# Kernel tuning notes

Hardware: AMD Instinct MI355X
Metric: run time of the kernel (lower is better)

Reference implementation:

```python
import jax, jax.numpy as jnp
import numpy as np

L = 32768          # sequence length (keys/values)
E = 1024           # embed_dim (hardcoded in module via weight slices)
H, D = 8, 128      # num_heads, head_dim (hardcoded via reshape(-1, 8, 128))


def setup_inputs() -> dict:
    key = jax.random.key(0)
    k1, k2, k3, k4, k5 = jax.random.split(key, 5)
    scale = 1.0 / np.sqrt(E)
    return {
        "x": jax.random.normal(k1, (L, E), dtype=jnp.float32),
        "in_proj_weight": jax.random.normal(k2, (3 * E, E), dtype=jnp.float32) * scale,
        "in_proj_bias": jax.random.normal(k3, (3 * E,), dtype=jnp.float32) * 0.02,
        "out_proj_weight": jax.random.normal(k4, (E, E), dtype=jnp.float32) * scale,
        "out_proj_bias": jax.random.normal(k5, (E,), dtype=jnp.float32) * 0.02,
    }


def reference(x, in_proj_weight, in_proj_bias, out_proj_weight, out_proj_bias):
    # Single-query (decode-style) attention: q from first token only.
    q = x[:1] @ in_proj_weight[:E].T + in_proj_bias[:E]              # [1, E]
    k = x @ in_proj_weight[E:2 * E].T + in_proj_bias[E:2 * E]        # [L, E]
    v = x @ in_proj_weight[2 * E:].T + in_proj_bias[2 * E:]          # [L, E]

    q = q.reshape(-1, H, D).transpose(1, 0, 2)                       # [H, 1, D]
    k = k.reshape(-1, H, D).transpose(1, 2, 0)                       # [H, D, L]
    v = v.reshape(-1, H, D).transpose(1, 0, 2)                       # [H, L, D]

    dot = jnp.matmul(q, k) * (1.0 / np.sqrt(D))                      # [H, 1, L]
    attn = jax.nn.softmax(dot, axis=-1)
    out = jnp.matmul(attn, v)                                        # [H, 1, D]

    out = out.transpose(1, 0, 2).reshape(-1, E)                      # [1, E]
    out = out @ out_proj_weight.T + out_proj_bias                    # [1, E]
    return out
```

## Files before the change

### kernel.cpp

```cpp
#include <hip/hip_runtime.h>
#include <math.h>


#define L_SEQ   32768
#define E_DIM   1024
#define NHEAD   8
#define HDIM    128
#define TILE_R  16
#define WAVES_M 8

__global__ __launch_bounds__(256) void proj_q(
    const float* __restrict__ W, const float* __restrict__ bias,
    const float* __restrict__ x, float* __restrict__ q)
{
  const int t = threadIdx.x, wave = t >> 6, lane = t & 63;
  const int o = blockIdx.x * 4 + wave;
  const float4* Wr = (const float4*)(W + (size_t)o * E_DIM);
  const float4* xr = (const float4*)x;
  float a = 0.f;
#pragma unroll
  for (int k = 0; k < 4; ++k) {
    float4 wv = Wr[lane + 64 * k];
    float4 xv = xr[lane + 64 * k];
    a += wv.x * xv.x + wv.y * xv.y + wv.z * xv.z + wv.w * xv.w;
  }
#pragma unroll
  for (int m = 1; m < 64; m <<= 1) a += __shfl_xor(a, m, 64);
  if (lane == 0) q[o] = a + bias[o];
}

__global__ __launch_bounds__(128) void make_p(
    const float* __restrict__ W, const float* __restrict__ q,
    float* __restrict__ P_T)
{
  const int h = blockIdx.y;
  const int e = blockIdx.x * 128 + threadIdx.x;
  const float* qh = q + h * HDIM;
  const float* Wb = W + ((size_t)E_DIM + (size_t)h * HDIM) * E_DIM + e;
  float a0 = 0.f, a1 = 0.f, a2 = 0.f, a3 = 0.f;
#pragma unroll 4
  for (int d = 0; d < HDIM; d += 4) {
    a0 += qh[d + 0] * Wb[(size_t)(d + 0) * E_DIM];
    a1 += qh[d + 1] * Wb[(size_t)(d + 1) * E_DIM];
    a2 += qh[d + 2] * Wb[(size_t)(d + 2) * E_DIM];
    a3 += qh[d + 3] * Wb[(size_t)(d + 3) * E_DIM];
  }
  P_T[h * E_DIM + e] = ((a0 + a1) + (a2 + a3)) * 0.08838834764831845f;
}

__global__ __launch_bounds__(512, 4) void attn_fused3(
    const float* __restrict__ x,
    const float* __restrict__ P_T,
    float* __restrict__ partial_z,
    float* __restrict__ partial_sumw,
    int rows_per_blk)
{
  __shared__ __align__(16) float P_lds[NHEAD * E_DIM];
  __shared__ __align__(16) float w_tile[2][TILE_R][NHEAD];
  __shared__ __align__(16) float sw_stage[WAVES_M][NHEAD];

  const int t = threadIdx.x;
  const int wave = t >> 6;
  const int lane = t & 63;
  const size_t row0 = (size_t)blockIdx.x * rows_per_blk;
  const int ntiles = rows_per_blk >> 4;

  const int rr_l = lane & 1;
  const int h_l = (((lane >> 1) & 1) << 2) | (((lane >> 2) & 1) << 1) | ((lane >> 3) & 1);

  {
    const float4* src = (const float4*)P_T;
    float4* dst = (float4*)P_lds;
#pragma unroll
    for (int i = 0; i < 4; ++i) dst[i * 512 + t] = src[i * 512 + t];
  }
  __syncthreads();

  float acc[16];
#pragma unroll
  for (int i = 0; i < 16; ++i) acc[i] = 0.f;
  float sumw_own = 0.f;

  for (int tile = 0; tile < ntiles; ++tile) {
    const int buf = tile & 1;
    const size_t trow = row0 + (size_t)tile * TILE_R;

    {
      const float4* xra = (const float4*)(x + (trow + wave * 2 + 0) * E_DIM);
      const float4* xrb = (const float4*)(x + (trow + wave * 2 + 1) * E_DIM);
      float4 xva[4], xvb[4];
#pragma unroll
      for (int k = 0; k < 4; ++k) xva[k] = xra[lane + 64 * k];
#pragma unroll
      for (int k = 0; k < 4; ++k) xvb[k] = xrb[lane + 64 * k];

      float v[16];
#pragma unroll
      for (int h = 0; h < NHEAD; ++h) {
        const float4* pr = (const float4*)(P_lds + h * E_DIM);
        float a0 = 0.f, a1 = 0.f;
#pragma unroll
        for (int k = 0; k < 4; ++k) {
          float4 p = pr[lane + 64 * k];
          a0 += xva[k].x * p.x + xva[k].y * p.y + xva[k].z * p.z + xva[k].w * p.w;
          a1 += xvb[k].x * p.x + xvb[k].y * p.y + xvb[k].z * p.z + xvb[k].w * p.w;
        }
        v[h] = a0; v[8 + h] = a1;
      }

#pragma unroll
      for (int lev = 0; lev < 4; ++lev) {
        const int d = 1 << lev;
        const int half = 8 >> lev;
#pragma unroll
        for (int i = 0; i < half; ++i) {
          float lo = v[i], hi = v[i + half];
          float keep = (lane & d) ? hi : lo;
          float oth  = (lane & d) ? lo : hi;
          v[i] = keep + __shfl_xor(oth, d, 64);
        }
      }
      float tot = v[0];
      tot += __shfl_xor(tot, 16, 64);
      tot += __shfl_xor(tot, 32, 64);

      const float w = __expf(tot);
      sumw_own += w;
      if (lane < 16) w_tile[buf][wave * 2 + rr_l][h_l] = w;
    }
    __syncthreads();

    {
      const float* xb = x + trow * E_DIM + 2 * t;
#pragma unroll
      for (int r4 = 0; r4 < TILE_R; r4 += 4) {
        float2 xv2[4];
#pragma unroll
        for (int j = 0; j < 4; ++j) xv2[j] = *(const float2*)(xb + (size_t)(r4 + j) * E_DIM);
        float4 wlo[4], whi[4];
#pragma unroll
        for (int j = 0; j < 4; ++j) {
          const float4* wp = (const float4*)&w_tile[buf][r4 + j][0];
          wlo[j] = wp[0]; whi[j] = wp[1];
        }
#pragma unroll
        for (int j = 0; j < 4; ++j) {
          acc[0]  += wlo[j].x * xv2[j].x;  acc[1]  += wlo[j].x * xv2[j].y;
          acc[2]  += wlo[j].y * xv2[j].x;  acc[3]  += wlo[j].y * xv2[j].y;
          acc[4]  += wlo[j].z * xv2[j].x;  acc[5]  += wlo[j].z * xv2[j].y;
          acc[6]  += wlo[j].w * xv2[j].x;  acc[7]  += wlo[j].w * xv2[j].y;
          acc[8]  += whi[j].x * xv2[j].x;  acc[9]  += whi[j].x * xv2[j].y;
          acc[10] += whi[j].y * xv2[j].x;  acc[11] += whi[j].y * xv2[j].y;
          acc[12] += whi[j].z * xv2[j].x;  acc[13] += whi[j].z * xv2[j].y;
          acc[14] += whi[j].w * xv2[j].x;  acc[15] += whi[j].w * xv2[j].y;
        }
      }
    }
  }

  {
    float* zd = partial_z + (size_t)blockIdx.x * (NHEAD * E_DIM) + 2 * t;
#pragma unroll
    for (int h = 0; h < NHEAD; ++h)
      *(float2*)(zd + h * E_DIM) = make_float2(acc[2 * h], acc[2 * h + 1]);
  }

  {
    float s2 = sumw_own + __shfl_xor(sumw_own, 1, 64);
    if (lane < 16 && (lane & 1) == 0) sw_stage[wave][h_l] = s2;
  }
  __syncthreads();
  if (t < NHEAD) {
    float s = 0.f;
#pragma unroll
    for (int wv = 0; wv < WAVES_M; ++wv) s += sw_stage[wv][t];
    partial_sumw[blockIdx.x * NHEAD + t] = s;
  }
}

__global__ __launch_bounds__(256) void reduce_z(
    const float* __restrict__ partial_z,
    const float* __restrict__ partial_sumw,
    float* __restrict__ zn, int nblk)
{
  __shared__ float red[256];
  __shared__ __align__(16) float swst[4][NHEAD];
  __shared__ float sumw_s[NHEAD];
  const int t = threadIdx.x;
  const int lane = t & 63, wave = t >> 6;

  float sw[NHEAD];
#pragma unroll
  for (int h = 0; h < NHEAD; ++h) sw[h] = 0.f;
  for (int b = t; b < nblk; b += 256) {
    const float4* p = (const float4*)(partial_sumw + (size_t)b * NHEAD);
    float4 a0 = p[0], a1 = p[1];
    sw[0] += a0.x; sw[1] += a0.y; sw[2] += a0.z; sw[3] += a0.w;
    sw[4] += a1.x; sw[5] += a1.y; sw[6] += a1.z; sw[7] += a1.w;
  }
#pragma unroll
  for (int m = 1; m < 64; m <<= 1) {
#pragma unroll
    for (int h = 0; h < NHEAD; ++h) sw[h] += __shfl_xor(sw[h], m, 64);
  }
  if (lane == 0) {
#pragma unroll
    for (int h = 0; h < NHEAD; ++h) swst[wave][h] = sw[h];
  }
  __syncthreads();
  if (t < NHEAD) sumw_s[t] = swst[0][t] + swst[1][t] + swst[2][t] + swst[3][t];

  const int o = blockIdx.x * 32 + (t & 31);
  const int g = t >> 5;
  float a = 0.f;
  for (int b = g; b < nblk; b += 8) a += partial_z[(size_t)b * (NHEAD * E_DIM) + o];
  red[t] = a;
  __syncthreads();
  if (t < 32) {
    float s2 = 0.f;
#pragma unroll
    for (int gg = 0; gg < 8; ++gg) s2 += red[gg * 32 + t];
    const int oo = blockIdx.x * 32 + t;
    zn[oo] = s2 / sumw_s[oo >> 10];
  }
}

__global__ __launch_bounds__(256) void proj_v(
    const float* __restrict__ W, const float* __restrict__ bias,
    const float* __restrict__ zn, float* __restrict__ attn)
{
  const int t = threadIdx.x, wave = t >> 6, lane = t & 63;
  const int o = blockIdx.x * 4 + wave;
  const float4* Wr = (const float4*)(W + ((size_t)2 * E_DIM + o) * E_DIM);
  const float4* zr = (const float4*)(zn + (size_t)(o >> 7) * E_DIM);
  float a = 0.f;
#pragma unroll
  for (int k = 0; k < 4; ++k) {
    float4 wv = Wr[lane + 64 * k];
    float4 zv = zr[lane + 64 * k];
    a += wv.x * zv.x + wv.y * zv.y + wv.z * zv.z + wv.w * zv.w;
  }
#pragma unroll
  for (int m = 1; m < 64; m <<= 1) a += __shfl_xor(a, m, 64);
  if (lane == 0) attn[o] = a + bias[2 * E_DIM + o];
}

__global__ __launch_bounds__(256) void proj_o(
    const float* __restrict__ Wo, const float* __restrict__ bo,
    const float* __restrict__ attn, float* __restrict__ out)
{
  const int t = threadIdx.x, wave = t >> 6, lane = t & 63;
  const int o = blockIdx.x * 4 + wave;
  const float4* Wr = (const float4*)(Wo + (size_t)o * E_DIM);
  const float4* vr = (const float4*)attn;
  float a = 0.f;
#pragma unroll
  for (int k = 0; k < 4; ++k) {
    float4 wv = Wr[lane + 64 * k];
    float4 vv = vr[lane + 64 * k];
    a += wv.x * vv.x + wv.y * vv.y + wv.z * vv.z + wv.w * vv.w;
  }
#pragma unroll
  for (int m = 1; m < 64; m <<= 1) a += __shfl_xor(a, m, 64);
  if (lane == 0) out[o] = a + bo[o];
}

extern "C" void kernel_launch(void* const* d_in, const int* in_sizes, int n_in,
                              void* d_out, int out_size, void* d_ws, size_t ws_size,
                              hipStream_t stream)
{
  const float* x  = (const float*)d_in[0];
  const float* Wi = (const float*)d_in[1];
  const float* bi = (const float*)d_in[2];
  const float* Wo = (const float*)d_in[3];
  const float* bo = (const float*)d_in[4];
  float* out = (float*)d_out;

  const size_t hdr = 90112;
  int nblk = 128;
  if (ws_size >= hdr + (size_t)512 * NHEAD * E_DIM * 4) nblk = 512;
  else if (ws_size >= hdr + (size_t)256 * NHEAD * E_DIM * 4) nblk = 256;
  const int rows_per_blk = L_SEQ / nblk;

  char* ws = (char*)d_ws;
  float* q     = (float*)(ws + 0);
  float* P_T   = (float*)(ws + 4096);
  float* zn    = (float*)(ws + 36864);
  float* attn  = (float*)(ws + 69632);
  float* psumw = (float*)(ws + 73728);
  float* pz    = (float*)(ws + hdr);

  proj_q     <<<256, 256, 0, stream>>>(Wi, bi, x, q);
  make_p     <<<dim3(8, 8), 128, 0, stream>>>(Wi, q, P_T);
  attn_fused3<<<nblk, 512, 0, stream>>>(x, P_T, pz, psumw, rows_per_blk);
  reduce_z   <<<256, 256, 0, stream>>>(pz, psumw, zn, nblk);
  proj_v     <<<256, 256, 0, stream>>>(Wi, bi, zn, attn);
  proj_o     <<<256, 256, 0, stream>>>(Wo, bo, attn, out);
}
```

Baseline: 243.1 us.

## Split fused attention kernel into score and accumulate passes with row prefetch

The fused kernel that computed exp-scores and then accumulated weighted x per 16-row tile with a barrier in between is split into two kernels. The score pass writes per-row weights to a global buffer and prefetches the next rows of x into registers, and it has no per-tile block barrier. The accumulate pass loads those weights into LDS and streams x with no barriers. The cost is reading the 128 MB x twice from memory instead of once, plus one extra launch, in exchange for removing per-tile synchronisation stalls.

```diff
diff --git a/kernel.cpp b/kernel.cpp
--- a/kernel.cpp
+++ b/kernel.cpp
@@ -6,7 +6,6 @@
 #define E_DIM   1024
 #define NHEAD   8
 #define HDIM    128
-#define TILE_R  16
 #define WAVES_M 8
 
 __global__ __launch_bounds__(256) void proj_q(
@@ -48,22 +47,21 @@
   P_T[h * E_DIM + e] = ((a0 + a1) + (a2 + a3)) * 0.08838834764831845f;
 }
 
-__global__ __launch_bounds__(512, 4) void attn_fused3(
+__global__ __launch_bounds__(512, 4) void score_pass(
     const float* __restrict__ x,
     const float* __restrict__ P_T,
-    float* __restrict__ partial_z,
+    float* __restrict__ wbuf,
     float* __restrict__ partial_sumw,
     int rows_per_blk)
 {
   __shared__ __align__(16) float P_lds[NHEAD * E_DIM];
-  __shared__ __align__(16) float w_tile[2][TILE_R][NHEAD];
   __shared__ __align__(16) float sw_stage[WAVES_M][NHEAD];
 
   const int t = threadIdx.x;
   const int wave = t >> 6;
   const int lane = t & 63;
   const size_t row0 = (size_t)blockIdx.x * rows_per_blk;
-  const int ntiles = rows_per_blk >> 4;
+  const int iters = rows_per_blk >> 4;
 
   const int rr_l = lane & 1;
   const int h_l = (((lane >> 1) & 1) << 2) | (((lane >> 2) & 1) << 1) | ((lane >> 3) & 1);
@@ -76,93 +74,71 @@
   }
   __syncthreads();
 
-  float acc[16];
-#pragma unroll
-  for (int i = 0; i < 16; ++i) acc[i] = 0.f;
   float sumw_own = 0.f;
 
-  for (int tile = 0; tile < ntiles; ++tile) {
-    const int buf = tile & 1;
-    const size_t trow = row0 + (size_t)tile * TILE_R;
-
-    {
-      const float4* xra = (const float4*)(x + (trow + wave * 2 + 0) * E_DIM);
-      const float4* xrb = (const float4*)(x + (trow + wave * 2 + 1) * E_DIM);
-      float4 xva[4], xvb[4];
-#pragma unroll
-      for (int k = 0; k < 4; ++k) xva[k] = xra[lane + 64 * k];
-#pragma unroll
-      for (int k = 0; k < 4; ++k) xvb[k] = xrb[lane + 64 * k];
-
-      float v[16];
-#pragma unroll
-      for (int h = 0; h < NHEAD; ++h) {
-        const float4* pr = (const float4*)(P_lds + h * E_DIM);
-        float a0 = 0.f, a1 = 0.f;
-#pragma unroll
-        for (int k = 0; k < 4; ++k) {
-          float4 p = pr[lane + 64 * k];
-          a0 += xva[k].x * p.x + xva[k].y * p.y + xva[k].z * p.z + xva[k].w * p.w;
-          a1 += xvb[k].x * p.x + xvb[k].y * p.y + xvb[k].z * p.z + xvb[k].w * p.w;
-        }
-        v[h] = a0; v[8 + h] = a1;
+  float4 xva[4], xvb[4];
+  {
+    const size_t trow = row0 + wave * 2;
+    const float4* xra = (const float4*)(x + trow * E_DIM);
+    const float4* xrb = (const float4*)(x + (trow + 1) * E_DIM);
+#pragma unroll
+    for (int k = 0; k < 4; ++k) xva[k] = xra[lane + 64 * k];
+#pragma unroll
+    for (int k = 0; k < 4; ++k) xvb[k] = xrb[lane + 64 * k];
+  }
+
+  for (int it = 0; it < iters; ++it) {
+    const size_t trow = row0 + (size_t)it * 16 + wave * 2;
+
+    float4 xna[4], xnb[4];
+    if (it + 1 < iters) {
+      const size_t nrow = trow + 16;
+      const float4* xra = (const float4*)(x + nrow * E_DIM);
+      const float4* xrb = (const float4*)(x + (nrow + 1) * E_DIM);
+#pragma unroll
+      for (int k = 0; k < 4; ++k) xna[k] = xra[lane + 64 * k];
+#pragma unroll
+      for (int k = 0; k < 4; ++k) xnb[k] = xrb[lane + 64 * k];
+    }
+
+    float v[16];
+#pragma unroll
+    for (int h = 0; h < NHEAD; ++h) {
+      const float4* pr = (const float4*)(P_lds + h * E_DIM);
+      float a0 = 0.f, a1 = 0.f;
+#pragma unroll
+      for (int k = 0; k < 4; ++k) {
+        float4 p = pr[lane + 64 * k];
+        a0 += xva[k].x * p.x + xva[k].y * p.y + xva[k].z * p.z + xva[k].w * p.w;
+        a1 += xvb[k].x * p.x + xvb[k].y * p.y + xvb[k].z * p.z + xvb[k].w * p.w;
       }
-
-#pragma unroll
-      for (int lev = 0; lev < 4; ++lev) {
-        const int d = 1 << lev;
-        const int half = 8 >> lev;
-#pragma unroll
-        for (int i = 0; i < half; ++i) {
-          float lo = v[i], hi = v[i + half];
-          float keep = (lane & d) ? hi : lo;
-          float oth  = (lane & d) ? lo : hi;
-          v[i] = keep + __shfl_xor(oth, d, 64);
-        }
+      v[h] = a0; v[8 + h] = a1;
+    }
+
+#pragma unroll
+    for (int lev = 0; lev < 4; ++lev) {
+      const int d = 1 << lev;
+      const int half = 8 >> lev;
+#pragma unroll
+      for (int i = 0; i < half; ++i) {
+        float lo = v[i], hi = v[i + half];
+        float keep = (lane & d) ? hi : lo;
+        float oth  = (lane & d) ? lo : hi;
+        v[i] = keep + __shfl_xor(oth, d, 64);
       }
-      float tot = v[0];
-      tot += __shfl_xor(tot, 16, 64);
-      tot += __shfl_xor(tot, 32, 64);
-
-      const float w = __expf(tot);
-      sumw_own += w;
-      if (lane < 16) w_tile[buf][wave * 2 + rr_l][h_l] = w;
-    }
-    __syncthreads();
-
-    {
-      const float* xb = x + trow * E_DIM + 2 * t;
-#pragma unroll
-      for (int r4 = 0; r4 < TILE_R; r4 += 4) {
-        float2 xv2[4];
-#pragma unroll
-        for (int j = 0; j < 4; ++j) xv2[j] = *(const float2*)(xb + (size_t)(r4 + j) * E_DIM);
-        float4 wlo[4], whi[4];
-#pragma unroll
-        for (int j = 0; j < 4; ++j) {
-          const float4* wp = (const float4*)&w_tile[buf][r4 + j][0];
-          wlo[j] = wp[0]; whi[j] = wp[1];
-        }
-#pragma unroll
-        for (int j = 0; j < 4; ++j) {
-          acc[0]  += wlo[j].x * xv2[j].x;  acc[1]  += wlo[j].x * xv2[j].y;
-          acc[2]  += wlo[j].y * xv2[j].x;  acc[3]  += wlo[j].y * xv2[j].y;
-          acc[4]  += wlo[j].z * xv2[j].x;  acc[5]  += wlo[j].z * xv2[j].y;
-          acc[6]  += wlo[j].w * xv2[j].x;  acc[7]  += wlo[j].w * xv2[j].y;
-          acc[8]  += whi[j].x * xv2[j].x;  acc[9]  += whi[j].x * xv2[j].y;
-          acc[10] += whi[j].y * xv2[j].x;  acc[11] += whi[j].y * xv2[j].y;
-          acc[12] += whi[j].z * xv2[j].x;  acc[13] += whi[j].z * xv2[j].y;
-          acc[14] += whi[j].w * xv2[j].x;  acc[15] += whi[j].w * xv2[j].y;
-        }
-      }
-    }
-  }
-
-  {
-    float* zd = partial_z + (size_t)blockIdx.x * (NHEAD * E_DIM) + 2 * t;
-#pragma unroll
-    for (int h = 0; h < NHEAD; ++h)
-      *(float2*)(zd + h * E_DIM) = make_float2(acc[2 * h], acc[2 * h + 1]);
+    }
+    float tot = v[0];
+    tot += __shfl_xor(tot, 16, 64);
+    tot += __shfl_xor(tot, 32, 64);
+
+    const float w = __expf(tot);
+    sumw_own += w;
+    if (lane < 16) wbuf[(trow + rr_l) * NHEAD + h_l] = w;
+
+    if (it + 1 < iters) {
+#pragma unroll
+      for (int k = 0; k < 4; ++k) { xva[k] = xna[k]; xvb[k] = xnb[k]; }
+    }
   }
 
   {
@@ -176,6 +152,54 @@
     for (int wv = 0; wv < WAVES_M; ++wv) s += sw_stage[wv][t];
     partial_sumw[blockIdx.x * NHEAD + t] = s;
   }
+}
+
+__global__ __launch_bounds__(512, 4) void accum_pass(
+    const float* __restrict__ x,
+    const float* __restrict__ wbuf,
+    float* __restrict__ partial_z,
+    int rows_per_blk)
+{
+  __shared__ __align__(16) float w_lds[2048];
+  const int t = threadIdx.x;
+  const size_t row0 = (size_t)blockIdx.x * rows_per_blk;
+
+  for (int i = t; i < rows_per_blk * NHEAD; i += 512)
+    w_lds[i] = wbuf[row0 * NHEAD + i];
+  __syncthreads();
+
+  float acc[16];
+#pragma unroll
+  for (int i = 0; i < 16; ++i) acc[i] = 0.f;
+
+  const float* xb = x + row0 * E_DIM + 2 * t;
+  for (int r4 = 0; r4 < rows_per_blk; r4 += 4) {
+    float2 xv2[4];
+#pragma unroll
+    for (int j = 0; j < 4; ++j) xv2[j] = *(const float2*)(xb + (size_t)(r4 + j) * E_DIM);
+    float4 wlo[4], whi[4];
+#pragma unroll
+    for (int j = 0; j < 4; ++j) {
+      const float4* wp = (const float4*)&w_lds[(r4 + j) * NHEAD];
+      wlo[j] = wp[0]; whi[j] = wp[1];
+    }
+#pragma unroll
+    for (int j = 0; j < 4; ++j) {
+      acc[0]  += wlo[j].x * xv2[j].x;  acc[1]  += wlo[j].x * xv2[j].y;
+      acc[2]  += wlo[j].y * xv2[j].x;  acc[3]  += wlo[j].y * xv2[j].y;
+      acc[4]  += wlo[j].z * xv2[j].x;  acc[5]  += wlo[j].z * xv2[j].y;
+      acc[6]  += wlo[j].w * xv2[j].x;  acc[7]  += wlo[j].w * xv2[j].y;
+      acc[8]  += whi[j].x * xv2[j].x;  acc[9]  += whi[j].x * xv2[j].y;
+      acc[10] += whi[j].y * xv2[j].x;  acc[11] += whi[j].y * xv2[j].y;
+      acc[12] += whi[j].z * xv2[j].x;  acc[13] += whi[j].z * xv2[j].y;
+      acc[14] += whi[j].w * xv2[j].x;  acc[15] += whi[j].w * xv2[j].y;
+    }
+  }
+
+  float* zd = partial_z + (size_t)blockIdx.x * (NHEAD * E_DIM) + 2 * t;
+#pragma unroll
+  for (int h = 0; h < NHEAD; ++h)
+    *(float2*)(zd + h * E_DIM) = make_float2(acc[2 * h], acc[2 * h + 1]);
 }
 
 __global__ __launch_bounds__(256) void reduce_z(
@@ -276,24 +300,26 @@
   const float* bo = (const float*)d_in[4];
   float* out = (float*)d_out;
 
-  const size_t hdr = 90112;
-  int nblk = 128;
-  if (ws_size >= hdr + (size_t)512 * NHEAD * E_DIM * 4) nblk = 512;
-  else if (ws_size >= hdr + (size_t)256 * NHEAD * E_DIM * 4) nblk = 256;
-  const int rows_per_blk = L_SEQ / nblk;
-
   char* ws = (char*)d_ws;
   float* q     = (float*)(ws + 0);
   float* P_T   = (float*)(ws + 4096);
   float* zn    = (float*)(ws + 36864);
   float* attn  = (float*)(ws + 69632);
   float* psumw = (float*)(ws + 73728);
-  float* pz    = (float*)(ws + hdr);
-
-  proj_q     <<<256, 256, 0, stream>>>(Wi, bi, x, q);
-  make_p     <<<dim3(8, 8), 128, 0, stream>>>(Wi, q, P_T);
-  attn_fused3<<<nblk, 512, 0, stream>>>(x, P_T, pz, psumw, rows_per_blk);
-  reduce_z   <<<256, 256, 0, stream>>>(pz, psumw, zn, nblk);
-  proj_v     <<<256, 256, 0, stream>>>(Wi, bi, zn, attn);
-  proj_o     <<<256, 256, 0, stream>>>(Wo, bo, attn, out);
-}
+  float* wbuf  = (float*)(ws + 90112);
+  const size_t pz_off = 1179648;
+  float* pz    = (float*)(ws + pz_off);
+
+  int nblk = 128;
+  if (ws_size >= pz_off + (size_t)512 * NHEAD * E_DIM * 4) nblk = 512;
+  else if (ws_size >= pz_off + (size_t)256 * NHEAD * E_DIM * 4) nblk = 256;
+  const int rows_per_blk = L_SEQ / nblk;
+
+  proj_q    <<<256, 256, 0, stream>>>(Wi, bi, x, q);
+  make_p    <<<dim3(8, 8), 128, 0, stream>>>(Wi, q, P_T);
+  score_pass<<<nblk, 512, 0, stream>>>(x, P_T, wbuf, psumw, rows_per_blk);
+  accum_pass<<<nblk, 512, 0, stream>>>(x, wbuf, pz, rows_per_blk);
+  reduce_z  <<<256, 256, 0, stream>>>(pz, psumw, zn, nblk);
+  proj_v    <<<256, 256, 0, stream>>>(Wi, bi, zn, attn);
+  proj_o    <<<256, 256, 0, stream>>>(Wo, bo, attn, out);
+}
```

Result: slower. 359.1 us (+47.7%).

## Stage x rows in LDS once and prefetch next row into registers

Applied to the files above, without the earlier changes.

The fused attention kernel used to read each x tile from global memory twice, once for the score dot products and again for the weighted accumulation. Now each wave loads one row into registers, writes it to an LDS tile for reuse by the accumulation phase, and prefetches the next row while it computes. The tile shrinks to 8 rows (one per wave) and the shuffle reduction is simplified to match. In exchange there is an extra barrier per tile, more LDS per block and a lower occupancy hint.

```diff
diff --git a/kernel.cpp b/kernel.cpp
--- a/kernel.cpp
+++ b/kernel.cpp
@@ -6,7 +6,7 @@
 #define E_DIM   1024
 #define NHEAD   8
 #define HDIM    128
-#define TILE_R  16
+#define TILE_R  8
 #define WAVES_M 8
 
 __global__ __launch_bounds__(256) void proj_q(
@@ -48,7 +48,7 @@
   P_T[h * E_DIM + e] = ((a0 + a1) + (a2 + a3)) * 0.08838834764831845f;
 }
 
-__global__ __launch_bounds__(512, 4) void attn_fused3(
+__global__ __launch_bounds__(512, 2) void attn_fused4(
     const float* __restrict__ x,
     const float* __restrict__ P_T,
     float* __restrict__ partial_z,
@@ -56,17 +56,17 @@
     int rows_per_blk)
 {
   __shared__ __align__(16) float P_lds[NHEAD * E_DIM];
-  __shared__ __align__(16) float w_tile[2][TILE_R][NHEAD];
+  __shared__ __align__(16) float x_tile[TILE_R][E_DIM];
+  __shared__ __align__(16) float w_tile[TILE_R][NHEAD];
   __shared__ __align__(16) float sw_stage[WAVES_M][NHEAD];
 
   const int t = threadIdx.x;
   const int wave = t >> 6;
   const int lane = t & 63;
   const size_t row0 = (size_t)blockIdx.x * rows_per_blk;
-  const int ntiles = rows_per_blk >> 4;
-
-  const int rr_l = lane & 1;
-  const int h_l = (((lane >> 1) & 1) << 2) | (((lane >> 2) & 1) << 1) | ((lane >> 3) & 1);
+  const int ntiles = rows_per_blk / TILE_R;
+
+  const int h_l = ((lane & 1) << 2) | (((lane >> 1) & 1) << 1) | ((lane >> 2) & 1);
 
   {
     const float4* src = (const float4*)P_T;
@@ -81,80 +81,85 @@
   for (int i = 0; i < 16; ++i) acc[i] = 0.f;
   float sumw_own = 0.f;
 
+  float4 xv[4];
+  {
+    const float4* xr = (const float4*)(x + (row0 + wave) * E_DIM);
+#pragma unroll
+    for (int k = 0; k < 4; ++k) xv[k] = xr[lane + 64 * k];
+  }
+
   for (int tile = 0; tile < ntiles; ++tile) {
-    const int buf = tile & 1;
     const size_t trow = row0 + (size_t)tile * TILE_R;
 
     {
-      const float4* xra = (const float4*)(x + (trow + wave * 2 + 0) * E_DIM);
-      const float4* xrb = (const float4*)(x + (trow + wave * 2 + 1) * E_DIM);
-      float4 xva[4], xvb[4];
-#pragma unroll
-      for (int k = 0; k < 4; ++k) xva[k] = xra[lane + 64 * k];
-#pragma unroll
-      for (int k = 0; k < 4; ++k) xvb[k] = xrb[lane + 64 * k];
-
-      float v[16];
-#pragma unroll
-      for (int h = 0; h < NHEAD; ++h) {
-        const float4* pr = (const float4*)(P_lds + h * E_DIM);
-        float a0 = 0.f, a1 = 0.f;
-#pragma unroll
-        for (int k = 0; k < 4; ++k) {
-          float4 p = pr[lane + 64 * k];
-          a0 += xva[k].x * p.x + xva[k].y * p.y + xva[k].z * p.z + xva[k].w * p.w;
-          a1 += xvb[k].x * p.x + xvb[k].y * p.y + xvb[k].z * p.z + xvb[k].w * p.w;
-        }
-        v[h] = a0; v[8 + h] = a1;
+      float4* xd = (float4*)&x_tile[wave][0];
+#pragma unroll
+      for (int k = 0; k < 4; ++k) xd[lane + 64 * k] = xv[k];
+    }
+
+    float4 xn[4];
+    if (tile + 1 < ntiles) {
+      const float4* xr = (const float4*)(x + (trow + TILE_R + wave) * E_DIM);
+#pragma unroll
+      for (int k = 0; k < 4; ++k) xn[k] = xr[lane + 64 * k];
+    }
+
+    float v[NHEAD];
+#pragma unroll
+    for (int h = 0; h < NHEAD; ++h) {
+      const float4* pr = (const float4*)(P_lds + h * E_DIM);
+      float a = 0.f;
+#pragma unroll
+      for (int k = 0; k < 4; ++k) {
+        float4 p = pr[lane + 64 * k];
+        a += xv[k].x * p.x + xv[k].y * p.y + xv[k].z * p.z + xv[k].w * p.w;
       }
-
-#pragma unroll
-      for (int lev = 0; lev < 4; ++lev) {
-        const int d = 1 << lev;
-        const int half = 8 >> lev;
-#pragma unroll
-        for (int i = 0; i < half; ++i) {
-          float lo = v[i], hi = v[i + half];
-          float keep = (lane & d) ? hi : lo;
-          float oth  = (lane & d) ? lo : hi;
-          v[i] = keep + __shfl_xor(oth, d, 64);
-        }
+      v[h] = a;
+    }
+
+#pragma unroll
+    for (int lev = 0; lev < 3; ++lev) {
+      const int d = 1 << lev;
+      const int half = 4 >> lev;
+#pragma unroll
+      for (int i = 0; i < half; ++i) {
+        float lo = v[i], hi = v[i + half];
+        float keep = (lane & d) ? hi : lo;
+        float oth  = (lane & d) ? lo : hi;
+        v[i] = keep + __shfl_xor(oth, d, 64);
       }
-      float tot = v[0];
-      tot += __shfl_xor(tot, 16, 64);
-      tot += __shfl_xor(tot, 32, 64);
-
-      const float w = __expf(tot);
-      sumw_own += w;
-      if (lane < 16) w_tile[buf][wave * 2 + rr_l][h_l] = w;
-    }
+    }
+    float tot = v[0];
+    tot += __shfl_xor(tot, 8, 64);
+    tot += __shfl_xor(tot, 16, 64);
+    tot += __shfl_xor(tot, 32, 64);
+
+    const float w = __expf(tot);
+    sumw_own += w;
+    if (lane < 8) w_tile[wave][h_l] = w;
+
     __syncthreads();
 
-    {
-      const float* xb = x + trow * E_DIM + 2 * t;
-#pragma unroll
-      for (int r4 = 0; r4 < TILE_R; r4 += 4) {
-        float2 xv2[4];
-#pragma unroll
-        for (int j = 0; j < 4; ++j) xv2[j] = *(const float2*)(xb + (size_t)(r4 + j) * E_DIM);
-        float4 wlo[4], whi[4];
-#pragma unroll
-        for (int j = 0; j < 4; ++j) {
-          const float4* wp = (const float4*)&w_tile[buf][r4 + j][0];
-          wlo[j] = wp[0]; whi[j] = wp[1];
-        }
-#pragma unroll
-        for (int j = 0; j < 4; ++j) {
-          acc[0]  += wlo[j].x * xv2[j].x;  acc[1]  += wlo[j].x * xv2[j].y;
-          acc[2]  += wlo[j].y * xv2[j].x;  acc[3]  += wlo[j].y * xv2[j].y;
-          acc[4]  += wlo[j].z * xv2[j].x;  acc[5]  += wlo[j].z * xv2[j].y;
-          acc[6]  += wlo[j].w * xv2[j].x;  acc[7]  += wlo[j].w * xv2[j].y;
-          acc[8]  += whi[j].x * xv2[j].x;  acc[9]  += whi[j].x * xv2[j].y;
-          acc[10] += whi[j].y * xv2[j].x;  acc[11] += whi[j].y * xv2[j].y;
-          acc[12] += whi[j].z * xv2[j].x;  acc[13] += whi[j].z * xv2[j].y;
-          acc[14] += whi[j].w * xv2[j].x;  acc[15] += whi[j].w * xv2[j].y;
-        }
-      }
+#pragma unroll
+    for (int r = 0; r < TILE_R; ++r) {
+      const float2 xv2 = *(const float2*)&x_tile[r][2 * t];
+      const float4* wp = (const float4*)&w_tile[r][0];
+      const float4 wlo = wp[0], whi = wp[1];
+      acc[0]  += wlo.x * xv2.x;  acc[1]  += wlo.x * xv2.y;
+      acc[2]  += wlo.y * xv2.x;  acc[3]  += wlo.y * xv2.y;
+      acc[4]  += wlo.z * xv2.x;  acc[5]  += wlo.z * xv2.y;
+      acc[6]  += wlo.w * xv2.x;  acc[7]  += wlo.w * xv2.y;
+      acc[8]  += whi.x * xv2.x;  acc[9]  += whi.x * xv2.y;
+      acc[10] += whi.y * xv2.x;  acc[11] += whi.y * xv2.y;
+      acc[12] += whi.z * xv2.x;  acc[13] += whi.z * xv2.y;
+      acc[14] += whi.w * xv2.x;  acc[15] += whi.w * xv2.y;
+    }
+
+    __syncthreads();
+
+    if (tile + 1 < ntiles) {
+#pragma unroll
+      for (int k = 0; k < 4; ++k) xv[k] = xn[k];
     }
   }
 
@@ -165,10 +170,7 @@
       *(float2*)(zd + h * E_DIM) = make_float2(acc[2 * h], acc[2 * h + 1]);
   }
 
-  {
-    float s2 = sumw_own + __shfl_xor(sumw_own, 1, 64);
-    if (lane < 16 && (lane & 1) == 0) sw_stage[wave][h_l] = s2;
-  }
+  if (lane < 8) sw_stage[wave][h_l] = sumw_own;
   __syncthreads();
   if (t < NHEAD) {
     float s = 0.f;
@@ -276,23 +278,23 @@
   const float* bo = (const float*)d_in[4];
   float* out = (float*)d_out;
 
-  const size_t hdr = 90112;
-  int nblk = 128;
-  if (ws_size >= hdr + (size_t)512 * NHEAD * E_DIM * 4) nblk = 512;
-  else if (ws_size >= hdr + (size_t)256 * NHEAD * E_DIM * 4) nblk = 256;
-  const int rows_per_blk = L_SEQ / nblk;
-
   char* ws = (char*)d_ws;
   float* q     = (float*)(ws + 0);
   float* P_T   = (float*)(ws + 4096);
   float* zn    = (float*)(ws + 36864);
   float* attn  = (float*)(ws + 69632);
   float* psumw = (float*)(ws + 73728);
-  float* pz    = (float*)(ws + hdr);
+  const size_t pz_off = 90112;
+  float* pz    = (float*)(ws + pz_off);
+
+  int nblk = 128;
+  if (ws_size >= pz_off + (size_t)512 * NHEAD * E_DIM * 4) nblk = 512;
+  else if (ws_size >= pz_off + (size_t)256 * NHEAD * E_DIM * 4) nblk = 256;
+  const int rows_per_blk = L_SEQ / nblk;
 
   proj_q     <<<256, 256, 0, stream>>>(Wi, bi, x, q);
   make_p     <<<dim3(8, 8), 128, 0, stream>>>(Wi, q, P_T);
-  attn_fused3<<<nblk, 512, 0, stream>>>(x, P_T, pz, psumw, rows_per_blk);
+  attn_fused4<<<nblk, 512, 0, stream>>>(x, P_T, pz, psumw, rows_per_blk);
   reduce_z   <<<256, 256, 0, stream>>>(pz, psumw, zn, nblk);
   proj_v     <<<256, 256, 0, stream>>>(Wi, bi, zn, attn);
   proj_o     <<<256, 256, 0, stream>>>(Wo, bo, attn, out);
```

Result: no change. 241.2 us (-0.8%).
